# Kernel tuning notes

Measured on AMD Instinct MI355X. Metric: run time of the kernel, lower is better.

## Reference

```python
import jax, jax.numpy as jnp
import numpy as np

DIM = 256; CTX_DIM = 256; K = 7; SK = 5; NH = 4  # num_heads*2
HD = DIM // NH; SCALE = HD ** -0.5
H = 64; W = 64; HC = 56; WC = 56
LN_EPS = 1e-6; BN_EPS = 1e-5


def make_bias_idx(k, h, w):
    # Faithful port of ContMix.generate_idx + apply_rpb index construction.
    rs = 2 * k - 1
    idx_h = np.arange(k); idx_w = np.arange(k)
    idx_k = (idx_h[:, None] * rs + idx_w).reshape(-1)
    rep_h = np.ones(k, np.int64); rep_h[k // 2] = h - (k - 1)
    rep_w = np.ones(k, np.int64); rep_w[k // 2] = w - (k - 1)
    bias_hw = np.repeat(idx_h, rep_h)[:, None] * rs + np.repeat(idx_w, rep_w)  # (h, w)
    bias_idx = (bias_hw[..., None] + idx_k).reshape(-1, k * k)                 # (h*w, k^2)
    return jnp.asarray(bias_idx[::-1].copy())  # torch.flip along dim 0


def window_idx(n, k):
    # NATTEN-style clamped neighborhood window starts.
    s = np.clip(np.arange(n) - k // 2, 0, n - k)
    return jnp.asarray(s[:, None] + np.arange(k))  # (n, k)


BIDX1 = make_bias_idx(SK, H, W)
BIDX2 = make_bias_idx(K, H, W)
IDXI_S = window_idx(H, SK); IDXJ_S = window_idx(W, SK)
IDXI_L = window_idx(H, K);  IDXJ_L = window_idx(W, K)


def ln2d(x, g, b):
    # LayerNorm over channel dim per spatial location, x: (B, C, H, W)
    mu = x.mean(1, keepdims=True)
    var = ((x - mu) ** 2).mean(1, keepdims=True)
    return (x - mu) * jax.lax.rsqrt(var + LN_EPS) * g[None, :, None, None] + b[None, :, None, None]


def conv1x1(x, Wt):
    return jnp.einsum('oc,bchw->bohw', Wt, x)


def apply_rpb(attn, rpb, bias_idx, h, w):
    g = rpb.shape[0]
    r = rpb.reshape(g, -1)[:, bias_idx]  # (g, h*w, k^2)
    return attn + r.reshape(1, g, h, w, -1)


def na2d_av(attn, value, k, idx_i, idx_j):
    # attn: (B, G, H, W, k^2), value: (B, G, H, W, C)
    B, G, h, w, _ = attn.shape
    v = value[:, :, idx_i]        # (B, G, H, k, W, C)
    v = v[:, :, :, :, idx_j]      # (B, G, H, k, W, k, C)
    a = attn.reshape(B, G, h, w, k, k)
    return jnp.einsum('bghwpq,bghpwqc->bghwc', a, v)


def contmix_forward(x, ctx, Wq, gq, bq, Wk, gk, bk, Wproj, rpb1, rpb2, Wdy, bn_g, bn_b):
    B = x.shape[0]
    q = ln2d(conv1x1(x, Wq), gq, bq) * SCALE                       # (B, DIM, H, W)
    # AdaptiveAvgPool2d(7) on 56x56 -> exact 8x8 bins
    kctx = ctx.reshape(B, CTX_DIM, 7, HC // 7, 7, WC // 7).mean((3, 5))
    kf = ln2d(conv1x1(kctx, Wk), gk, bk)                            # (B, DIM, 7, 7)
    q = q.reshape(B, NH, HD, H * W)
    kf = kf.reshape(B, NH, HD, 49)
    wgt = jnp.einsum('bgcn,bgcl->bgnl', q, kf)                      # (B, 4, HW, 49)
    wgt = jnp.einsum('ml,bgnl->bgnm', Wproj, wgt)                   # (B, 4, HW, 74)
    wgt = wgt.reshape(B, NH, H, W, SK * SK + K * K)
    attn1 = wgt[:, :NH // 2, :, :, :SK * SK]                        # group1, 25
    attn2 = wgt[:, NH // 2:, :, :, SK * SK:]                        # group2, 49
    attn1 = jax.nn.softmax(apply_rpb(attn1, rpb1, BIDX1, H, W), -1)
    attn2 = jax.nn.softmax(apply_rpb(attn2, rpb2, BIDX2, H, W), -1)
    # 'b (m g c) h w -> m b g h w c', m=2, g=2
    v = x.reshape(B, 2, NH // 2, HD, H, W).transpose(1, 0, 2, 4, 5, 3)
    x1 = na2d_av(attn1, v[0], SK, IDXI_S, IDXJ_S)                   # (B, 2, H, W, HD)
    x2 = na2d_av(attn2, v[1], K, IDXI_L, IDXJ_L)
    out = jnp.concatenate([x1, x2], axis=1)                         # (B, 4, H, W, HD)
    out = out.transpose(0, 1, 4, 2, 3).reshape(B, DIM, H, W)
    out = conv1x1(out, Wdy)
    # BatchNorm2d in eval mode: running_mean=0, running_var=1
    out = out * (bn_g * jax.lax.rsqrt(jnp.float32(1.0) + BN_EPS))[None, :, None, None] + bn_b[None, :, None, None]
    return out


def setup_inputs() -> dict:
    key = jax.random.key(0)
    ks = jax.random.split(key, 10)
    d = {}
    d['x'] = jax.random.normal(ks[0], (4, DIM, H, W), jnp.float32)
    d['ctx'] = jax.random.normal(ks[1], (4, CTX_DIM, HC, WC), jnp.float32)
    d['Wq'] = jax.random.normal(ks[2], (DIM, DIM), jnp.float32) * 0.02
    d['gq'] = jnp.ones((DIM,), jnp.float32)
    d['bq'] = jnp.zeros((DIM,), jnp.float32)
    d['Wk'] = jax.random.normal(ks[3], (DIM, CTX_DIM), jnp.float32) * 0.02
    d['gk'] = jnp.ones((DIM,), jnp.float32)
    d['bk'] = jnp.zeros((DIM,), jnp.float32)
    d['Wproj'] = jax.random.normal(ks[4], (SK * SK + K * K, 49), jnp.float32) * 0.1
    d['rpb1'] = jax.random.normal(ks[5], (NH // 2, 2 * SK - 1, 2 * SK - 1), jnp.float32) * 0.02
    d['rpb2'] = jax.random.normal(ks[6], (NH // 2, 2 * K - 1, 2 * K - 1), jnp.float32) * 0.02
    d['Wdy'] = jax.random.normal(ks[7], (DIM, DIM), jnp.float32) * 0.02
    d['bn_g'] = jnp.ones((DIM,), jnp.float32)
    d['bn_b'] = jnp.zeros((DIM,), jnp.float32)
    return d


def reference(x, ctx, Wq, gq, bq, Wk, gk, bk, Wproj, rpb1, rpb2, Wdy, bn_g, bn_b):
    return contmix_forward(x, ctx, Wq, gq, bq, Wk, gk, bk, Wproj, rpb1, rpb2, Wdy, bn_g, bn_b)
```

## Files before the change

kernel.cpp:

```cpp
#include <hip/hip_runtime.h>

#define DEV __device__ __forceinline__

typedef __bf16 bf16x8 __attribute__((ext_vector_type(8)));
typedef __bf16 bf16x4 __attribute__((ext_vector_type(4)));
typedef float floatx4 __attribute__((ext_vector_type(4)));

__global__ __launch_bounds__(256)
void prep_kernel(const float* __restrict__ Wq, const float* __restrict__ Wdy,
                 const float* __restrict__ ctx, const float* __restrict__ x,
                 __bf16* __restrict__ wqb, __bf16* __restrict__ wdyb,
                 float* __restrict__ kctx, __bf16* __restrict__ xt,
                 float* __restrict__ stats) {
  __shared__ float tile[64][65];
  int bid = blockIdx.x, t = threadIdx.x;
  if (bid < 256) {
    int i = bid * 256 + t;
    wqb[i]  = (__bf16)Wq[i];
    wdyb[i] = (__bf16)Wdy[i];
  } else if (bid < 512) {
    int bc = (bid - 256) * 4 + (t >> 6);
    const float* src = ctx + (size_t)bc * (56 * 56);
    int w = t & 63;
#pragma unroll
    for (int pi = 0; pi < 7; ++pi) {
      float s = 0.f;
      if (w < 56) {
#pragma unroll
        for (int di = 0; di < 8; ++di) s += src[(pi * 8 + di) * 56 + w];
      }
      s += __shfl_down(s, 4);
      s += __shfl_down(s, 2);
      s += __shfl_down(s, 1);
      if (w < 56 && (w & 7) == 0)
        kctx[(size_t)bc * 49 + pi * 7 + (w >> 3)] = s * (1.f / 64.f);
    }
  } else if (bid < 1536) {
    int idx = bid - 512;
    int b = idx >> 8, c0 = ((idx >> 6) & 3) * 64, n0 = (idx & 63) * 64;
    int lane = t & 63, rg = t >> 6;
    const float* src = x + ((size_t)b * 256 + c0) * 4096 + n0;
    for (int i = rg; i < 64; i += 4) tile[i][lane] = src[(size_t)i * 4096 + lane];
    __syncthreads();
    __bf16* dst = xt + ((size_t)b * 4096 + n0) * 256 + c0;
    for (int i = rg; i < 64; i += 4) dst[(size_t)i * 256 + lane] = (__bf16)tile[lane][i];
  } else {
    int base = (bid - 1536) * 1024 + t * 4;
    *(float4*)&stats[base] = make_float4(0.f, 0.f, 0.f, 0.f);
  }
}

__global__ __launch_bounds__(256)
void kf_ln_kernel(const float* __restrict__ kctx, const float* __restrict__ Wk,
                  const float* __restrict__ gk, const float* __restrict__ bk,
                  float* __restrict__ kf) {
  int b = blockIdx.x / 49, l = blockIdx.x % 49;
  __shared__ float xs[256];
  __shared__ float r1[4], r2[4];
  int o = threadIdx.x;
  xs[o] = kctx[((size_t)b * 256 + o) * 49 + l];
  __syncthreads();
  const float* wrow = Wk + (size_t)o * 256;
  float acc = 0.f;
#pragma unroll 8
  for (int c = 0; c < 256; c += 4) {
    float4 wv = *(const float4*)(wrow + c);
    acc += wv.x * xs[c] + wv.y * xs[c + 1] + wv.z * xs[c + 2] + wv.w * xs[c + 3];
  }
  float s1 = acc, s2 = acc * acc;
#pragma unroll
  for (int off = 32; off > 0; off >>= 1) {
    s1 += __shfl_down(s1, off);
    s2 += __shfl_down(s2, off);
  }
  int wv_ = o >> 6, ln = o & 63;
  if (ln == 0) { r1[wv_] = s1; r2[wv_] = s2; }
  __syncthreads();
  float mu  = (r1[0] + r1[1] + r1[2] + r1[3]) * (1.f / 256.f);
  float var = (r2[0] + r2[1] + r2[2] + r2[3]) * (1.f / 256.f) - mu * mu;
  float rstd = rsqrtf(var + 1e-6f);
  kf[((size_t)b * 256 + o) * 49 + l] = (acc - mu) * rstd * gk[o] + bk[o];
}

__global__ __launch_bounds__(256)
void kfp_kernel(const float* __restrict__ kf, const float* __restrict__ Wproj,
                __bf16* __restrict__ kfpT) {
  int bg = blockIdx.x; int b = bg >> 2, g = bg & 3;
  int m0 = blockIdx.y * 16;
  __shared__ float kfs[64][50];
  __shared__ float wps[16][50];
  int t = threadIdx.x;
  for (int i = t; i < 64 * 49; i += 256) {
    int d = i / 49, l = i % 49;
    kfs[d][l] = kf[((size_t)b * 256 + g * 64 + d) * 49 + l];
  }
  for (int i = t; i < 16 * 49; i += 256) {
    int m = i / 49, l = i % 49;
    wps[m][l] = (m0 + m < 74) ? Wproj[(m0 + m) * 49 + l] : 0.f;
  }
  __syncthreads();
  for (int i = t; i < 64 * 16; i += 256) {
    int d = i >> 4, m = i & 15;
    float s = 0.f;
    if (m0 + m < 74) {
#pragma unroll 7
      for (int l = 0; l < 49; ++l) s += kfs[d][l] * wps[m][l];
    }
    kfpT[(size_t)bg * 5120 + (m0 + m) * 64 + d] = (__bf16)s;
  }
}

template <int MODE>
__global__ __launch_bounds__(256, 2)
void conv_mfma_kernel(const __bf16* __restrict__ Wb, const __bf16* __restrict__ Xin,
                      void* __restrict__ Yout, float* __restrict__ stats,
                      const float* __restrict__ bn_g, const float* __restrict__ bn_b) {
  int b  = blockIdx.z;
  int n0 = blockIdx.x * 128;
  int o0 = blockIdx.y * 128;
  __shared__ __bf16 As[128 * 32];
  __shared__ __bf16 Bs[128 * 32];
  int t = threadIdx.x;
  int lane = t & 63, wv = t >> 6;
  int mq = (wv & 1) * 64, nq = (wv >> 1) * 64;
  int col = lane & 15, quad = lane >> 4;
  floatx4 acc[4][4];
#pragma unroll
  for (int i = 0; i < 4; ++i)
#pragma unroll
    for (int j = 0; j < 4; ++j) acc[i][j] = {0.f, 0.f, 0.f, 0.f};
  int sm = t >> 1, sk = (t & 1) << 4;
  for (int c0 = 0; c0 < 256; c0 += 32) {
    const __bf16* wsrc = Wb + (size_t)(o0 + sm) * 256 + c0 + sk;
    *(bf16x8*)&As[sm * 32 + sk]     = *(const bf16x8*)wsrc;
    *(bf16x8*)&As[sm * 32 + sk + 8] = *(const bf16x8*)(wsrc + 8);
    const __bf16* xsrc;
    if (MODE == 0) {
      xsrc = Xin + ((size_t)b * 4096 + n0 + sm) * 256 + c0 + sk;
    } else {
      int c = c0 + sk, g = c >> 6, c64 = c & 63;
      xsrc = Xin + (((size_t)(b * 4 + g)) * 4096 + n0 + sm) * 64 + c64;
    }
    *(bf16x8*)&Bs[sm * 32 + sk]     = *(const bf16x8*)xsrc;
    *(bf16x8*)&Bs[sm * 32 + sk + 8] = *(const bf16x8*)(xsrc + 8);
    __syncthreads();
    bf16x8 fa[4], fb[4];
#pragma unroll
    for (int i = 0; i < 4; ++i)
      fa[i] = *(const bf16x8*)&As[(mq + i * 16 + col) * 32 + quad * 8];
#pragma unroll
    for (int j = 0; j < 4; ++j)
      fb[j] = *(const bf16x8*)&Bs[(nq + j * 16 + col) * 32 + quad * 8];
#pragma unroll
    for (int i = 0; i < 4; ++i)
#pragma unroll
      for (int j = 0; j < 4; ++j)
        acc[i][j] = __builtin_amdgcn_mfma_f32_16x16x32_bf16(fa[i], fb[j], acc[i][j], 0, 0, 0);
    __syncthreads();
  }
  if (MODE == 0) {
    __bf16* QT = (__bf16*)Yout + (size_t)b * 4096 * 256;
    float s_j[4] = {0.f, 0.f, 0.f, 0.f}, q_j[4] = {0.f, 0.f, 0.f, 0.f};
#pragma unroll
    for (int i = 0; i < 4; ++i) {
#pragma unroll
      for (int j = 0; j < 4; ++j) {
        int o = o0 + mq + i * 16 + quad * 4;
        int n = n0 + nq + j * 16 + col;
        __bf16 pk[4];
#pragma unroll
        for (int r = 0; r < 4; ++r) {
          float v = acc[i][j][r];
          s_j[j] += v; q_j[j] += v * v;
          pk[r] = (__bf16)v;
        }
        *(bf16x4*)&QT[(size_t)n * 256 + o] = *(bf16x4*)pk;
      }
    }
#pragma unroll
    for (int j = 0; j < 4; ++j) {
      float s = s_j[j], qq = q_j[j];
      s  += __shfl_down(s, 32);  s  += __shfl_down(s, 16);
      qq += __shfl_down(qq, 32); qq += __shfl_down(qq, 16);
      if (quad == 0) {
        int n = n0 + nq + j * 16 + col;
        atomicAdd(&stats[(size_t)b * 4096 + n], s);
        atomicAdd(&stats[16384 + (size_t)b * 4096 + n], qq);
      }
    }
  } else {
    float* Yf = (float*)Yout + (size_t)b * 256 * 4096;
#pragma unroll
    for (int i = 0; i < 4; ++i) {
#pragma unroll
      for (int r = 0; r < 4; ++r) {
        int o = o0 + mq + i * 16 + quad * 4 + r;
        float scale = bn_g[o] * 0.9999950000374997f;
        float shift = bn_b[o];
        float* yrow = Yf + (size_t)o * 4096 + n0 + nq + col;
#pragma unroll
        for (int j = 0; j < 4; ++j) yrow[j * 16] = acc[i][j][r] * scale + shift;
      }
    }
  }
}

DEV int rep_idx(int p, int kc, int t1, int sub) {
  return p < kc ? p : (p < t1 ? kc : p - sub);
}

template <int KK>
DEV void softmax_write(const float* wms, const float* rpb_s, __bf16* __restrict__ attnL,
                       int bg, int n_glob, int t) {
  constexpr int CNT = KK * KK;
  constexpr int RS  = 2 * KK - 1;
  constexpr int KC  = KK / 2;
  constexpr int T1  = KC + (64 - KK + 1);
  constexpr int SUB = 64 - KK;
  constexpr int MLO = (KK == 5) ? 0 : 25;
  constexpr int PW  = (KK == 5) ? 32 : 56;
  int h = n_glob >> 6, w = n_glob & 63;
  int rh = rep_idx(63 - h, KC, T1, SUB);
  int rw = rep_idx(63 - w, KC, T1, SUB);
  float vals[CNT];
  float mx = -1e30f;
#pragma unroll
  for (int m = 0; m < CNT; ++m) {
    int ki = m / KK, kj = m % KK;
    float v = wms[t * 81 + MLO + m] + rpb_s[(rh + ki) * RS + rw + kj];
    vals[m] = v; mx = fmaxf(mx, v);
  }
  float ssum = 0.f;
#pragma unroll
  for (int m = 0; m < CNT; ++m) { float e = __expf(vals[m] - mx); vals[m] = e; ssum += e; }
  float inv = 1.f / ssum;
  __bf16 hv[PW];
#pragma unroll
  for (int m = 0; m < PW; ++m) hv[m] = (__bf16)(m < CNT ? vals[m] * inv : 0.f);
  __bf16* ap = attnL + ((size_t)bg * 4096 + n_glob) * 56;
#pragma unroll
  for (int i = 0; i < PW / 8; ++i) *(bf16x8*)(ap + i * 8) = *(bf16x8*)&hv[i * 8];
}

__global__ __launch_bounds__(256)
void attn_kernel(const __bf16* __restrict__ qT, const float* __restrict__ stats,
                 const float* __restrict__ gq, const float* __restrict__ bq,
                 const __bf16* __restrict__ kfpT, const float* __restrict__ rpb1,
                 const float* __restrict__ rpb2, __bf16* __restrict__ attnL) {
  __shared__ uint32_t smem4[10368];
  __shared__ float rpb_s[169];
  __bf16* A_s = (__bf16*)smem4;
  __bf16* B_s = (__bf16*)smem4 + 9216;
  float* wms  = (float*)smem4;
  int bg = blockIdx.x; int b = bg >> 2, g = bg & 3;
  int n0 = blockIdx.y * 128;
  int t = threadIdx.x;
  for (int idx = t; idx < 1024; idx += 256) {
    int n = idx >> 3, d8 = idx & 7;
    int ng = n0 + n;
    float s  = stats[(size_t)b * 4096 + ng];
    float ss = stats[16384 + (size_t)b * 4096 + ng];
    float mu = s * (1.f / 256.f);
    float rs = rsqrtf(ss * (1.f / 256.f) - mu * mu + 1e-6f);
    bf16x8 raw = *(const bf16x8*)&qT[((size_t)b * 4096 + ng) * 256 + g * 64 + d8 * 8];
    __bf16 tmp[8];
#pragma unroll
    for (int e = 0; e < 8; ++e) {
      int d = g * 64 + d8 * 8 + e;
      tmp[e] = (__bf16)((((float)raw[e]) - mu) * rs * (gq[d] * 0.125f) + bq[d] * 0.125f);
    }
    *(bf16x8*)&A_s[n * 72 + d8 * 8] = *(bf16x8*)tmp;
  }
  for (int idx = t; idx < 640; idx += 256)
    *(bf16x8*)&B_s[(idx >> 3) * 72 + (idx & 7) * 8] = *(const bf16x8*)&kfpT[(size_t)bg * 5120 + idx * 8];
  if (g < 2) { for (int i = t; i <  81; i += 256) rpb_s[i] = rpb1[g * 81 + i]; }
  else       { for (int i = t; i < 169; i += 256) rpb_s[i] = rpb2[(g - 2) * 169 + i]; }
  __syncthreads();
  int lane = t & 63, wv = t >> 6;
  int col = lane & 15, quad = lane >> 4;
  floatx4 acc[2][5];
#pragma unroll
  for (int mi = 0; mi < 2; ++mi)
#pragma unroll
    for (int nt = 0; nt < 5; ++nt) acc[mi][nt] = {0.f, 0.f, 0.f, 0.f};
  bf16x8 fa[2][2], fb[2][5];
#pragma unroll
  for (int ks = 0; ks < 2; ++ks) {
#pragma unroll
    for (int mi = 0; mi < 2; ++mi)
      fa[ks][mi] = *(const bf16x8*)&A_s[((wv * 2 + mi) * 16 + col) * 72 + ks * 32 + quad * 8];
#pragma unroll
    for (int nt = 0; nt < 5; ++nt)
      fb[ks][nt] = *(const bf16x8*)&B_s[(nt * 16 + col) * 72 + ks * 32 + quad * 8];
  }
#pragma unroll
  for (int ks = 0; ks < 2; ++ks)
#pragma unroll
    for (int mi = 0; mi < 2; ++mi)
#pragma unroll
      for (int nt = 0; nt < 5; ++nt)
        acc[mi][nt] = __builtin_amdgcn_mfma_f32_16x16x32_bf16(fa[ks][mi], fb[ks][nt], acc[mi][nt], 0, 0, 0);
  __syncthreads();
#pragma unroll
  for (int mi = 0; mi < 2; ++mi)
#pragma unroll
    for (int nt = 0; nt < 5; ++nt)
#pragma unroll
      for (int r = 0; r < 4; ++r)
        wms[((wv * 2 + mi) * 16 + quad * 4 + r) * 81 + nt * 16 + col] = acc[mi][nt][r];
  __syncthreads();
  if (t < 128) {
    int n_glob = n0 + t;
    if (g < 2) softmax_write<5>(wms, rpb_s, attnL, bg, n_glob, t);
    else       softmax_write<7>(wms, rpb_s, attnL, bg, n_glob, t);
  }
}

template <int KK>
DEV void na2d_body(const __bf16* __restrict__ attnL, const __bf16* __restrict__ XT,
                   __bf16* __restrict__ midT, __bf16* xs, int bg, int h0, int chalf, int t) {
  constexpr int CNT = KK * KK, KC = KK / 2, SMAX = 64 - KK;
  constexpr int ROWS = KK + 3;
  constexpr int PW = (KK == 5) ? 32 : 56;
  int b = bg >> 2, g = bg & 3;
  int si0 = min(max(h0 - KC, 0), SMAX);
  {
    int sn = t >> 2, sc = t & 3;
    const __bf16* src = XT + ((size_t)b * 4096 + sn) * 256 + g * 64 + chalf * 32 + sc * 8;
#pragma unroll
    for (int r = 0; r < ROWS; ++r) {
      int gr = min(si0 + r, 63);
      *(bf16x8*)&xs[(r * 64 + sn) * 40 + sc * 8] = *(const bf16x8*)(src + (size_t)gr * 64 * 256);
    }
  }
  __syncthreads();
  int w = t >> 2, cg = t & 3;
  int sj = min(max(w - KC, 0), SMAX);
#pragma unroll
  for (int h4 = 0; h4 < 4; ++h4) {
    int h = h0 + h4;
    int base = min(max(h - KC, 0), SMAX) - si0;
    bf16x8 avh[PW / 8];
    const __bf16* ap = attnL + ((size_t)bg * 4096 + h * 64 + w) * 56;
#pragma unroll
    for (int i = 0; i < PW / 8; ++i) avh[i] = *(const bf16x8*)(ap + i * 8);
    float av[CNT];
#pragma unroll
    for (int m = 0; m < CNT; ++m) av[m] = (float)avh[m / 8][m % 8];
    float acc[8] = {};
#pragma unroll
    for (int p = 0; p < KK; ++p) {
      const __bf16* xr = &xs[((base + p) * 64 + sj) * 40 + cg * 8];
#pragma unroll
      for (int q = 0; q < KK; ++q) {
        bf16x8 v = *(const bf16x8*)(xr + q * 40);
        float a = av[p * KK + q];
#pragma unroll
        for (int e = 0; e < 8; ++e) acc[e] += a * (float)v[e];
      }
    }
    __bf16 hv[8];
#pragma unroll
    for (int e = 0; e < 8; ++e) hv[e] = (__bf16)acc[e];
    *(bf16x8*)&midT[((size_t)bg * 4096 + h * 64 + w) * 64 + chalf * 32 + cg * 8] = *(bf16x8*)hv;
  }
}

__global__ __launch_bounds__(256)
void na2d_kernel(const __bf16* __restrict__ attnL, const __bf16* __restrict__ XT,
                 __bf16* __restrict__ midT) {
  __shared__ __bf16 xs[10 * 64 * 40];
  int bg = blockIdx.x, h0 = blockIdx.y * 4, chalf = blockIdx.z, t = threadIdx.x;
  if ((bg & 3) < 2) na2d_body<5>(attnL, XT, midT, xs, bg, h0, chalf, t);
  else              na2d_body<7>(attnL, XT, midT, xs, bg, h0, chalf, t);
}

extern "C" void kernel_launch(void* const* d_in, const int* in_sizes, int n_in,
                              void* d_out, int out_size, void* d_ws, size_t ws_size,
                              hipStream_t stream) {
  const float* x     = (const float*)d_in[0];
  const float* ctx   = (const float*)d_in[1];
  const float* Wq    = (const float*)d_in[2];
  const float* gq    = (const float*)d_in[3];
  const float* bq    = (const float*)d_in[4];
  const float* Wk    = (const float*)d_in[5];
  const float* gk    = (const float*)d_in[6];
  const float* bk    = (const float*)d_in[7];
  const float* Wproj = (const float*)d_in[8];
  const float* rpb1  = (const float*)d_in[9];
  const float* rpb2  = (const float*)d_in[10];
  const float* Wdy   = (const float*)d_in[11];
  const float* bn_g  = (const float*)d_in[12];
  const float* bn_b  = (const float*)d_in[13];
  float* out = (float*)d_out;

  float* ws     = (float*)d_ws;
  float* kctx   = ws;
  float* kf     = kctx + 50176;
  float* stats  = kf + 50176;
  __bf16* attnL = (__bf16*)(stats + 32768);
  __bf16* wqb   = attnL + 3670016;
  __bf16* wdyb  = wqb + 65536;
  __bf16* kfpT  = wdyb + 65536;
  __bf16* XT    = kfpT + 81920;
  __bf16* qT    = XT + 4194304;
  __bf16* midT  = qT + 4194304;

  prep_kernel<<<dim3(1568), dim3(256), 0, stream>>>(Wq, Wdy, ctx, x, wqb, wdyb, kctx, XT, stats);
  kf_ln_kernel<<<dim3(196), dim3(256), 0, stream>>>(kctx, Wk, gk, bk, kf);
  kfp_kernel<<<dim3(16, 5), dim3(256), 0, stream>>>(kf, Wproj, kfpT);
  conv_mfma_kernel<0><<<dim3(32, 2, 4), dim3(256), 0, stream>>>(wqb, XT, qT, stats, nullptr, nullptr);
  attn_kernel<<<dim3(16, 32), dim3(256), 0, stream>>>(qT, stats, gq, bq, kfpT, rpb1, rpb2, attnL);
  na2d_kernel<<<dim3(16, 16, 2), dim3(256), 0, stream>>>(attnL, XT, midT);
  conv_mfma_kernel<1><<<dim3(32, 2, 4), dim3(256), 0, stream>>>(wdyb, midT, out, nullptr, bn_g, bn_b);
}
```

Measured before the change: 166.2 us.

## Fuse q projection, LayerNorm and attention logits into one kernel

Replaces the q-conv GEMM plus separate attention kernel with a single kernel. Each block computes all 256 output channels for 64 pixels, so LayerNorm statistics are reduced in shared memory, with no atomics, no stats buffer and no qT round trip through global memory. It then runs the kfp GEMM and softmax in place, using register-prefetched global loads for the GEMM. The trade-off is 256 blocks at one block per CU with large shared memory (about 85KB), which limits occupancy.

```diff
diff --git a/kernel.cpp b/kernel.cpp
--- a/kernel.cpp
+++ b/kernel.cpp
@@ -10,8 +10,7 @@
 void prep_kernel(const float* __restrict__ Wq, const float* __restrict__ Wdy,
                  const float* __restrict__ ctx, const float* __restrict__ x,
                  __bf16* __restrict__ wqb, __bf16* __restrict__ wdyb,
-                 float* __restrict__ kctx, __bf16* __restrict__ xt,
-                 float* __restrict__ stats) {
+                 float* __restrict__ kctx, __bf16* __restrict__ xt) {
   __shared__ float tile[64][65];
   int bid = blockIdx.x, t = threadIdx.x;
   if (bid < 256) {
@@ -35,7 +34,7 @@
       if (w < 56 && (w & 7) == 0)
         kctx[(size_t)bc * 49 + pi * 7 + (w >> 3)] = s * (1.f / 64.f);
     }
-  } else if (bid < 1536) {
+  } else {
     int idx = bid - 512;
     int b = idx >> 8, c0 = ((idx >> 6) & 3) * 64, n0 = (idx & 63) * 64;
     int lane = t & 63, rg = t >> 6;
@@ -44,9 +43,6 @@
     __syncthreads();
     __bf16* dst = xt + ((size_t)b * 4096 + n0) * 256 + c0;
     for (int i = rg; i < 64; i += 4) dst[(size_t)i * 256 + lane] = (__bf16)tile[lane][i];
-  } else {
-    int base = (bid - 1536) * 1024 + t * 4;
-    *(float4*)&stats[base] = make_float4(0.f, 0.f, 0.f, 0.f);
   }
 }
 
@@ -108,6 +104,202 @@
     }
     kfpT[(size_t)bg * 5120 + (m0 + m) * 64 + d] = (__bf16)s;
   }
+}
+
+DEV int rep_idx(int p, int kc, int t1, int sub) {
+  return p < kc ? p : (p < t1 ? kc : p - sub);
+}
+
+template <int KK>
+DEV void softmax_write(const float* wms, const float* rpb_s, __bf16* __restrict__ attnL,
+                       int bg, int n_glob, int t) {
+  constexpr int CNT = KK * KK;
+  constexpr int RS  = 2 * KK - 1;
+  constexpr int KC  = KK / 2;
+  constexpr int T1  = KC + (64 - KK + 1);
+  constexpr int SUB = 64 - KK;
+  constexpr int MLO = (KK == 5) ? 0 : 25;
+  constexpr int PW  = (KK == 5) ? 32 : 56;
+  int h = n_glob >> 6, w = n_glob & 63;
+  int rh = rep_idx(63 - h, KC, T1, SUB);
+  int rw = rep_idx(63 - w, KC, T1, SUB);
+  float vals[CNT];
+  float mx = -1e30f;
+#pragma unroll
+  for (int m = 0; m < CNT; ++m) {
+    int ki = m / KK, kj = m % KK;
+    float v = wms[t * 81 + MLO + m] + rpb_s[(rh + ki) * RS + rw + kj];
+    vals[m] = v; mx = fmaxf(mx, v);
+  }
+  float ssum = 0.f;
+#pragma unroll
+  for (int m = 0; m < CNT; ++m) { float e = __expf(vals[m] - mx); vals[m] = e; ssum += e; }
+  float inv = 1.f / ssum;
+  __bf16 hv[PW];
+#pragma unroll
+  for (int m = 0; m < PW; ++m) hv[m] = (__bf16)(m < CNT ? vals[m] * inv : 0.f);
+  __bf16* ap = attnL + ((size_t)bg * 4096 + n_glob) * 56;
+#pragma unroll
+  for (int i = 0; i < PW / 8; ++i) *(bf16x8*)(ap + i * 8) = *(bf16x8*)&hv[i * 8];
+}
+
+__global__ __launch_bounds__(256, 1)
+void qattn_kernel(const __bf16* __restrict__ Wb, const __bf16* __restrict__ XT,
+                  const __bf16* __restrict__ kfpT,
+                  const float* __restrict__ gq, const float* __restrict__ bq,
+                  const float* __restrict__ rpb1, const float* __restrict__ rpb2,
+                  __bf16* __restrict__ attnL) {
+  __shared__ float wms[256 * 81];
+  __shared__ float rpb_s[500];
+  __shared__ float gqs[256], bqs[256];
+  __shared__ float red_s[256], red_q[256];
+  __shared__ float st_mu[64], st_rs[64];
+  __bf16* As  = (__bf16*)wms;
+  __bf16* Bs  = (__bf16*)wms + 8192;
+  __bf16* Aat = (__bf16*)wms;
+
+  int b  = blockIdx.z;
+  int n0 = blockIdx.x * 64;
+  int t  = threadIdx.x;
+  int lane = t & 63, wv = t >> 6;
+  int col = lane & 15, quad = lane >> 4;
+
+  gqs[t] = gq[t] * 0.125f;
+  bqs[t] = bq[t] * 0.125f;
+  for (int i = t; i < 162; i += 256) rpb_s[i] = rpb1[i];
+  for (int i = t; i < 338; i += 256) rpb_s[162 + i] = rpb2[i];
+
+  floatx4 acc[4][4];
+#pragma unroll
+  for (int i = 0; i < 4; ++i)
+#pragma unroll
+    for (int j = 0; j < 4; ++j) acc[i][j] = {0.f, 0.f, 0.f, 0.f};
+
+  int rowA = t >> 1, halfA = (t & 1) * 16;
+  int rowB = t >> 2, kB = (t & 3) * 8;
+  const __bf16* wp  = Wb + (size_t)rowA * 256 + halfA;
+  const __bf16* wp2 = wp + 128 * 256;
+  const __bf16* xp  = XT + ((size_t)b * 4096 + n0 + rowB) * 256 + kB;
+  bf16x8 ra0a = *(const bf16x8*)wp;
+  bf16x8 ra0b = *(const bf16x8*)(wp + 8);
+  bf16x8 ra1a = *(const bf16x8*)wp2;
+  bf16x8 ra1b = *(const bf16x8*)(wp2 + 8);
+  bf16x8 rb   = *(const bf16x8*)xp;
+
+  for (int c0 = 0; c0 < 256; c0 += 32) {
+    *(bf16x8*)&As[rowA * 32 + halfA]             = ra0a;
+    *(bf16x8*)&As[rowA * 32 + halfA + 8]         = ra0b;
+    *(bf16x8*)&As[(128 + rowA) * 32 + halfA]     = ra1a;
+    *(bf16x8*)&As[(128 + rowA) * 32 + halfA + 8] = ra1b;
+    *(bf16x8*)&Bs[rowB * 32 + kB]                = rb;
+    __syncthreads();
+    if (c0 + 32 < 256) {
+      ra0a = *(const bf16x8*)(wp  + c0 + 32);
+      ra0b = *(const bf16x8*)(wp  + c0 + 40);
+      ra1a = *(const bf16x8*)(wp2 + c0 + 32);
+      ra1b = *(const bf16x8*)(wp2 + c0 + 40);
+      rb   = *(const bf16x8*)(xp  + c0 + 32);
+    }
+    bf16x8 fa[4], fb[4];
+#pragma unroll
+    for (int i = 0; i < 4; ++i)
+      fa[i] = *(const bf16x8*)&As[(wv * 64 + i * 16 + col) * 32 + quad * 8];
+#pragma unroll
+    for (int j = 0; j < 4; ++j)
+      fb[j] = *(const bf16x8*)&Bs[(j * 16 + col) * 32 + quad * 8];
+#pragma unroll
+    for (int i = 0; i < 4; ++i)
+#pragma unroll
+      for (int j = 0; j < 4; ++j)
+        acc[i][j] = __builtin_amdgcn_mfma_f32_16x16x32_bf16(fa[i], fb[j], acc[i][j], 0, 0, 0);
+    __syncthreads();
+  }
+
+  float sj[4], qj[4];
+#pragma unroll
+  for (int j = 0; j < 4; ++j) {
+    float s = 0.f, q = 0.f;
+#pragma unroll
+    for (int i = 0; i < 4; ++i)
+#pragma unroll
+      for (int r = 0; r < 4; ++r) { float v = acc[i][j][r]; s += v; q += v * v; }
+    s += __shfl_xor(s, 16); s += __shfl_xor(s, 32);
+    q += __shfl_xor(q, 16); q += __shfl_xor(q, 32);
+    sj[j] = s; qj[j] = q;
+  }
+  if (quad == 0) {
+#pragma unroll
+    for (int j = 0; j < 4; ++j) {
+      red_s[wv * 64 + j * 16 + col] = sj[j];
+      red_q[wv * 64 + j * 16 + col] = qj[j];
+    }
+  }
+  __syncthreads();
+  if (t < 64) {
+    float s = red_s[t] + red_s[64 + t] + red_s[128 + t] + red_s[192 + t];
+    float q = red_q[t] + red_q[64 + t] + red_q[128 + t] + red_q[192 + t];
+    float mu  = s * (1.f / 256.f);
+    float var = q * (1.f / 256.f) - mu * mu;
+    st_mu[t] = mu;
+    st_rs[t] = rsqrtf(var + 1e-6f);
+  }
+  __syncthreads();
+
+#pragma unroll
+  for (int j = 0; j < 4; ++j) {
+    float mu = st_mu[j * 16 + col], rs = st_rs[j * 16 + col];
+#pragma unroll
+    for (int i = 0; i < 4; ++i) {
+      __bf16 pk[4];
+#pragma unroll
+      for (int r = 0; r < 4; ++r) {
+        int o = wv * 64 + i * 16 + quad * 4 + r;
+        pk[r] = (__bf16)((acc[i][j][r] - mu) * rs * gqs[o] + bqs[o]);
+      }
+      *(bf16x4*)&Aat[(wv * 64 + j * 16 + col) * 72 + i * 16 + quad * 4] = *(bf16x4*)pk;
+    }
+  }
+  __syncthreads();
+
+  bf16x8 fa2[2][4], fb2[2][5];
+  const __bf16* kp = kfpT + (size_t)(b * 4 + wv) * 5120;
+#pragma unroll
+  for (int ks = 0; ks < 2; ++ks) {
+#pragma unroll
+    for (int a = 0; a < 4; ++a)
+      fa2[ks][a] = *(const bf16x8*)&Aat[(wv * 64 + a * 16 + col) * 72 + ks * 32 + quad * 8];
+#pragma unroll
+    for (int nt = 0; nt < 5; ++nt)
+      fb2[ks][nt] = *(const bf16x8*)&kp[(nt * 16 + col) * 64 + ks * 32 + quad * 8];
+  }
+  floatx4 acc2[4][5];
+#pragma unroll
+  for (int a = 0; a < 4; ++a)
+#pragma unroll
+    for (int nt = 0; nt < 5; ++nt) acc2[a][nt] = {0.f, 0.f, 0.f, 0.f};
+#pragma unroll
+  for (int ks = 0; ks < 2; ++ks)
+#pragma unroll
+    for (int a = 0; a < 4; ++a)
+#pragma unroll
+      for (int nt = 0; nt < 5; ++nt)
+        acc2[a][nt] = __builtin_amdgcn_mfma_f32_16x16x32_bf16(fa2[ks][a], fb2[ks][nt], acc2[a][nt], 0, 0, 0);
+  __syncthreads();
+
+#pragma unroll
+  for (int a = 0; a < 4; ++a)
+#pragma unroll
+    for (int nt = 0; nt < 5; ++nt)
+#pragma unroll
+      for (int r = 0; r < 4; ++r)
+        wms[(wv * 64 + a * 16 + quad * 4 + r) * 81 + nt * 16 + col] = acc2[a][nt][r];
+  __syncthreads();
+
+  int g2 = t >> 6;
+  int n_glob = n0 + (t & 63);
+  int bg = b * 4 + g2;
+  if (g2 < 2) softmax_write<5>(wms, rpb_s + g2 * 81,              attnL, bg, n_glob, t);
+  else        softmax_write<7>(wms, rpb_s + 162 + (g2 - 2) * 169, attnL, bg, n_glob, t);
 }
 
 template <int MODE>
@@ -158,37 +350,7 @@
         acc[i][j] = __builtin_amdgcn_mfma_f32_16x16x32_bf16(fa[i], fb[j], acc[i][j], 0, 0, 0);
     __syncthreads();
   }
-  if (MODE == 0) {
-    __bf16* QT = (__bf16*)Yout + (size_t)b * 4096 * 256;
-    float s_j[4] = {0.f, 0.f, 0.f, 0.f}, q_j[4] = {0.f, 0.f, 0.f, 0.f};
-#pragma unroll
-    for (int i = 0; i < 4; ++i) {
-#pragma unroll
-      for (int j = 0; j < 4; ++j) {
-        int o = o0 + mq + i * 16 + quad * 4;
-        int n = n0 + nq + j * 16 + col;
-        __bf16 pk[4];
-#pragma unroll
-        for (int r = 0; r < 4; ++r) {
-          float v = acc[i][j][r];
-          s_j[j] += v; q_j[j] += v * v;
-          pk[r] = (__bf16)v;
-        }
-        *(bf16x4*)&QT[(size_t)n * 256 + o] = *(bf16x4*)pk;
-      }
-    }
-#pragma unroll
-    for (int j = 0; j < 4; ++j) {
-      float s = s_j[j], qq = q_j[j];
-      s  += __shfl_down(s, 32);  s  += __shfl_down(s, 16);
-      qq += __shfl_down(qq, 32); qq += __shfl_down(qq, 16);
-      if (quad == 0) {
-        int n = n0 + nq + j * 16 + col;
-        atomicAdd(&stats[(size_t)b * 4096 + n], s);
-        atomicAdd(&stats[16384 + (size_t)b * 4096 + n], qq);
-      }
-    }
-  } else {
+  {
     float* Yf = (float*)Yout + (size_t)b * 256 * 4096;
 #pragma unroll
     for (int i = 0; i < 4; ++i) {
@@ -202,117 +364,6 @@
         for (int j = 0; j < 4; ++j) yrow[j * 16] = acc[i][j][r] * scale + shift;
       }
     }
-  }
-}
-
-DEV int rep_idx(int p, int kc, int t1, int sub) {
-  return p < kc ? p : (p < t1 ? kc : p - sub);
-}
-
-template <int KK>
-DEV void softmax_write(const float* wms, const float* rpb_s, __bf16* __restrict__ attnL,
-                       int bg, int n_glob, int t) {
-  constexpr int CNT = KK * KK;
-  constexpr int RS  = 2 * KK - 1;
-  constexpr int KC  = KK / 2;
-  constexpr int T1  = KC + (64 - KK + 1);
-  constexpr int SUB = 64 - KK;
-  constexpr int MLO = (KK == 5) ? 0 : 25;
-  constexpr int PW  = (KK == 5) ? 32 : 56;
-  int h = n_glob >> 6, w = n_glob & 63;
-  int rh = rep_idx(63 - h, KC, T1, SUB);
-  int rw = rep_idx(63 - w, KC, T1, SUB);
-  float vals[CNT];
-  float mx = -1e30f;
-#pragma unroll
-  for (int m = 0; m < CNT; ++m) {
-    int ki = m / KK, kj = m % KK;
-    float v = wms[t * 81 + MLO + m] + rpb_s[(rh + ki) * RS + rw + kj];
-    vals[m] = v; mx = fmaxf(mx, v);
-  }
-  float ssum = 0.f;
-#pragma unroll
-  for (int m = 0; m < CNT; ++m) { float e = __expf(vals[m] - mx); vals[m] = e; ssum += e; }
-  float inv = 1.f / ssum;
-  __bf16 hv[PW];
-#pragma unroll
-  for (int m = 0; m < PW; ++m) hv[m] = (__bf16)(m < CNT ? vals[m] * inv : 0.f);
-  __bf16* ap = attnL + ((size_t)bg * 4096 + n_glob) * 56;
-#pragma unroll
-  for (int i = 0; i < PW / 8; ++i) *(bf16x8*)(ap + i * 8) = *(bf16x8*)&hv[i * 8];
-}
-
-__global__ __launch_bounds__(256)
-void attn_kernel(const __bf16* __restrict__ qT, const float* __restrict__ stats,
-                 const float* __restrict__ gq, const float* __restrict__ bq,
-                 const __bf16* __restrict__ kfpT, const float* __restrict__ rpb1,
-                 const float* __restrict__ rpb2, __bf16* __restrict__ attnL) {
-  __shared__ uint32_t smem4[10368];
-  __shared__ float rpb_s[169];
-  __bf16* A_s = (__bf16*)smem4;
-  __bf16* B_s = (__bf16*)smem4 + 9216;
-  float* wms  = (float*)smem4;
-  int bg = blockIdx.x; int b = bg >> 2, g = bg & 3;
-  int n0 = blockIdx.y * 128;
-  int t = threadIdx.x;
-  for (int idx = t; idx < 1024; idx += 256) {
-    int n = idx >> 3, d8 = idx & 7;
-    int ng = n0 + n;
-    float s  = stats[(size_t)b * 4096 + ng];
-    float ss = stats[16384 + (size_t)b * 4096 + ng];
-    float mu = s * (1.f / 256.f);
-    float rs = rsqrtf(ss * (1.f / 256.f) - mu * mu + 1e-6f);
-    bf16x8 raw = *(const bf16x8*)&qT[((size_t)b * 4096 + ng) * 256 + g * 64 + d8 * 8];
-    __bf16 tmp[8];
-#pragma unroll
-    for (int e = 0; e < 8; ++e) {
-      int d = g * 64 + d8 * 8 + e;
-      tmp[e] = (__bf16)((((float)raw[e]) - mu) * rs * (gq[d] * 0.125f) + bq[d] * 0.125f);
-    }
-    *(bf16x8*)&A_s[n * 72 + d8 * 8] = *(bf16x8*)tmp;
-  }
-  for (int idx = t; idx < 640; idx += 256)
-    *(bf16x8*)&B_s[(idx >> 3) * 72 + (idx & 7) * 8] = *(const bf16x8*)&kfpT[(size_t)bg * 5120 + idx * 8];
-  if (g < 2) { for (int i = t; i <  81; i += 256) rpb_s[i] = rpb1[g * 81 + i]; }
-  else       { for (int i = t; i < 169; i += 256) rpb_s[i] = rpb2[(g - 2) * 169 + i]; }
-  __syncthreads();
-  int lane = t & 63, wv = t >> 6;
-  int col = lane & 15, quad = lane >> 4;
-  floatx4 acc[2][5];
-#pragma unroll
-  for (int mi = 0; mi < 2; ++mi)
-#pragma unroll
-    for (int nt = 0; nt < 5; ++nt) acc[mi][nt] = {0.f, 0.f, 0.f, 0.f};
-  bf16x8 fa[2][2], fb[2][5];
-#pragma unroll
-  for (int ks = 0; ks < 2; ++ks) {
-#pragma unroll
-    for (int mi = 0; mi < 2; ++mi)
-      fa[ks][mi] = *(const bf16x8*)&A_s[((wv * 2 + mi) * 16 + col) * 72 + ks * 32 + quad * 8];
-#pragma unroll
-    for (int nt = 0; nt < 5; ++nt)
-      fb[ks][nt] = *(const bf16x8*)&B_s[(nt * 16 + col) * 72 + ks * 32 + quad * 8];
-  }
-#pragma unroll
-  for (int ks = 0; ks < 2; ++ks)
-#pragma unroll
-    for (int mi = 0; mi < 2; ++mi)
-#pragma unroll
-      for (int nt = 0; nt < 5; ++nt)
-        acc[mi][nt] = __builtin_amdgcn_mfma_f32_16x16x32_bf16(fa[ks][mi], fb[ks][nt], acc[mi][nt], 0, 0, 0);
-  __syncthreads();
-#pragma unroll
-  for (int mi = 0; mi < 2; ++mi)
-#pragma unroll
-    for (int nt = 0; nt < 5; ++nt)
-#pragma unroll
-      for (int r = 0; r < 4; ++r)
-        wms[((wv * 2 + mi) * 16 + quad * 4 + r) * 81 + nt * 16 + col] = acc[mi][nt][r];
-  __syncthreads();
-  if (t < 128) {
-    int n_glob = n0 + t;
-    if (g < 2) softmax_write<5>(wms, rpb_s, attnL, bg, n_glob, t);
-    else       softmax_write<7>(wms, rpb_s, attnL, bg, n_glob, t);
   }
 }
 
@@ -397,20 +448,17 @@
   float* ws     = (float*)d_ws;
   float* kctx   = ws;
   float* kf     = kctx + 50176;
-  float* stats  = kf + 50176;
-  __bf16* attnL = (__bf16*)(stats + 32768);
+  __bf16* attnL = (__bf16*)(kf + 50176);
   __bf16* wqb   = attnL + 3670016;
   __bf16* wdyb  = wqb + 65536;
   __bf16* kfpT  = wdyb + 65536;
   __bf16* XT    = kfpT + 81920;
-  __bf16* qT    = XT + 4194304;
-  __bf16* midT  = qT + 4194304;
-
-  prep_kernel<<<dim3(1568), dim3(256), 0, stream>>>(Wq, Wdy, ctx, x, wqb, wdyb, kctx, XT, stats);
+  __bf16* midT  = XT + 4194304;
+
+  prep_kernel<<<dim3(1536), dim3(256), 0, stream>>>(Wq, Wdy, ctx, x, wqb, wdyb, kctx, XT);
   kf_ln_kernel<<<dim3(196), dim3(256), 0, stream>>>(kctx, Wk, gk, bk, kf);
   kfp_kernel<<<dim3(16, 5), dim3(256), 0, stream>>>(kf, Wproj, kfpT);
-  conv_mfma_kernel<0><<<dim3(32, 2, 4), dim3(256), 0, stream>>>(wqb, XT, qT, stats, nullptr, nullptr);
-  attn_kernel<<<dim3(16, 32), dim3(256), 0, stream>>>(qT, stats, gq, bq, kfpT, rpb1, rpb2, attnL);
+  qattn_kernel<<<dim3(64, 1, 4), dim3(256), 0, stream>>>(wqb, XT, kfpT, gq, bq, rpb1, rpb2, attnL);
   na2d_kernel<<<dim3(16, 16, 2), dim3(256), 0, stream>>>(attnL, XT, midT);
   conv_mfma_kernel<1><<<dim3(32, 2, 4), dim3(256), 0, stream>>>(wdyb, midT, out, nullptr, bn_g, bn_b);
 }
```

After: 162.1 us. 1.03x faster.
